# Kernel tuning notes

Hardware: AMD Instinct MI355X
Metric: run time of the kernel (lower is better)

Reference implementation:

```python
import jax, jax.numpy as jnp
import numpy as np

H = 256          # hidden_channels
R = 64           # num_rbf
N = 20000        # nodes
E = 320000       # edges
CUTOFF_LO = 0.0
CUTOFF_UP = 5.0
LN_EPS = 1e-5


def _layernorm(x, g, b):
    mu = jnp.mean(x, axis=-1, keepdims=True)
    var = jnp.var(x, axis=-1, keepdims=True)
    return (x - mu) * jax.lax.rsqrt(var + LN_EPS) * g + b


def _cosine_cutoff(r):
    # cutoff_lower == 0 branch of CosineCutoff
    c = 0.5 * (jnp.cos(r * (jnp.pi / CUTOFF_UP)) + 1.0)
    return c * (r < CUTOFF_UP).astype(r.dtype)


def setup_inputs() -> dict:
    key = jax.random.key(0)
    ks = jax.random.split(key, 16)
    def xavier(k, shape):
        fan_in, fan_out = shape[1], shape[0]
        lim = np.sqrt(6.0 / (fan_in + fan_out))
        return jax.random.uniform(k, shape, jnp.float32, -lim, lim)
    x = jax.random.normal(ks[0], (N, H), jnp.float32)
    edge_index = jax.random.randint(ks[1], (2, E), 0, N, jnp.int64)
    edge_weight = jax.random.uniform(ks[2], (E,), jnp.float32, 0.0, CUTOFF_UP)
    edge_attr = jax.random.normal(ks[3], (E, R), jnp.float32)
    return {
        "x": x,
        "edge_index": edge_index,
        "edge_weight": edge_weight,
        "edge_attr": edge_attr,
        "ln_g": jnp.ones((H,), jnp.float32),
        "ln_b": jnp.zeros((H,), jnp.float32),
        "Wq": xavier(ks[4], (H, H)), "bq": jnp.zeros((H,), jnp.float32),
        "Wk": xavier(ks[5], (H, H)), "bk": jnp.zeros((H,), jnp.float32),
        "Wv": xavier(ks[6], (H, H)), "bv": jnp.zeros((H,), jnp.float32),
        "Wo": xavier(ks[7], (H, H)), "bo": jnp.zeros((H,), jnp.float32),
        "Wdk": xavier(ks[8], (H, R)), "bdk": jnp.zeros((H,), jnp.float32),
        "Wdv": xavier(ks[9], (H, R)), "bdv": jnp.zeros((H,), jnp.float32),
    }


def reference(x, edge_index, edge_weight, edge_attr,
              ln_g, ln_b, Wq, bq, Wk, bk, Wv, bv, Wo, bo, Wdk, bdk, Wdv, bdv):
    src = edge_index[0]  # j (messages come from)
    dst = edge_index[1]  # i (messages aggregate to)

    x_norm = _layernorm(x, ln_g, ln_b)                     # [N,H]
    q = x_norm @ Wq.T + bq                                 # [N,H]
    k = x_norm @ Wk.T + bk
    v = x_norm @ Wv.T + bv

    dk = jax.nn.silu(edge_attr @ Wdk.T + bdk)              # [E,H]
    dv = jax.nn.silu(edge_attr @ Wdv.T + bdv)              # [E,H]

    q_i = q[dst]                                           # [E,H]
    k_j = k[src]
    v_j = v[src]

    attn = jnp.sum(q_i * k_j * dk, axis=1)                 # [E]
    attn = jax.nn.silu(attn) * _cosine_cutoff(edge_weight) # [E]

    msg = v_j * dv * attn[:, None]                         # [E,H]
    agg = jax.ops.segment_sum(msg, dst, num_segments=x.shape[0])  # [N,H]

    out = agg @ Wo.T + bo
    return x + out
```

## Files before the change

### kernel.cpp

```cpp
#include <hip/hip_runtime.h>
#include <math.h>

#define NN 20000
#define H 256
#define R 64
#define EE 320000
#define LN_EPS 1e-5f
#define NB 79

using short8  = __attribute__((ext_vector_type(8))) short;
using ushort8 = __attribute__((ext_vector_type(8))) unsigned short;
using f32x4   = __attribute__((ext_vector_type(4))) float;

typedef __attribute__((address_space(3))) unsigned int lds_uint;
typedef const __attribute__((address_space(1))) unsigned int glb_uint;

__device__ __forceinline__ float silu_f(float x) {
    return x * __builtin_amdgcn_rcpf(1.0f + __expf(-x));
}

__device__ __forceinline__ unsigned short f2bf(float f) {
    unsigned u = __float_as_uint(f);
    u += 0x7fff + ((u >> 16) & 1);
    return (unsigned short)(u >> 16);
}
__device__ __forceinline__ float bf2f(unsigned short s) {
    return __uint_as_float(((unsigned)s) << 16);
}
__device__ __forceinline__ unsigned short f2h(float f) {
    unsigned r;
    asm("v_cvt_f16_f32 %0, %1" : "=v"(r) : "v"(f));
    return (unsigned short)r;
}
__device__ __forceinline__ float h2f(unsigned short h) {
    float f;
    asm("v_cvt_f32_f16 %0, %1" : "=v"(f) : "v"((unsigned)h));
    return f;
}

__device__ __forceinline__ int sw_idx(int row, int col) {
    return row * 64 + ((((col >> 3) ^ (row & 7)) << 3) | (col & 7));
}
__device__ __forceinline__ int dh_idx(int row, int col) {
    return row * 128 + (col ^ (((row >> 2) & 3) << 4));
}

__global__ __launch_bounds__(256) void k_prep(
    const float* __restrict__ Wq, const float* __restrict__ Wk,
    const float* __restrict__ Wv, const float* __restrict__ Wo,
    const float* __restrict__ g,  const float* __restrict__ b,
    const float* __restrict__ bq, const float* __restrict__ bk, const float* __restrict__ bv,
    const float* __restrict__ Wdk, const float* __restrict__ Wdv,
    unsigned short* __restrict__ wqkv_p, unsigned short* __restrict__ wo_p,
    unsigned short* __restrict__ wdk_p,  unsigned short* __restrict__ wdv_p,
    float* __restrict__ bias3, int* __restrict__ hist)
{
    const int bid = blockIdx.x, t = threadIdx.x;
    if (bid < 128) {
        const int mat = bid >> 5;
        const float* W = mat == 0 ? Wq : (mat == 1 ? Wk : (mat == 2 ? Wv : Wo));
        unsigned short* out = (mat < 3) ? wqkv_p + (size_t)mat * 131072 : wo_p;
        const int fold = mat < 3;
        const int flat = (bid & 31) * 256 + t;
        const int tile = flat >> 9;
        const int rem  = flat & 511;
        const int ks   = rem >> 6;
        const int lane = rem & 63;
        const int nl = lane & 15, quad = lane >> 4;
        const int h  = tile * 16 + nl;
        const int c0 = ks * 32 + quad * 8;
        short8 hi8, lo8;
        #pragma unroll
        for (int j = 0; j < 8; ++j) {
            float wv = W[(size_t)h * 256 + c0 + j];
            if (fold) wv *= g[c0 + j];
            const unsigned short hh = f2bf(wv);
            hi8[j] = (short)hh;
            lo8[j] = (short)f2bf(wv - bf2f(hh));
        }
        unsigned short* ob = out + ((size_t)(tile * 8 + ks)) * 1024;
        *(short8*)&ob[lane * 8] = hi8;
        *(short8*)&ob[512 + lane * 8] = lo8;
    } else if (bid < 160) {
        const int flat = (bid - 128) * 256 + t;
        const int mat  = flat >> 12;
        const int rem  = flat & 4095;
        const int hh   = rem >> 11;
        const int r2   = rem & 2047;
        const int row  = r2 >> 4;
        const int col4 = (r2 & 15) * 4;
        const float* W = mat == 0 ? Wdk : Wdv;
        unsigned short* out = (mat == 0 ? wdk_p : wdv_p) + hh * 16384;
        const float4 w4 = *(const float4*)(W + (size_t)(hh * 128 + row) * 64 + col4);
        const unsigned short h0 = f2bf(w4.x), h1 = f2bf(w4.y), h2 = f2bf(w4.z), h3 = f2bf(w4.w);
        ushort4 hi4 = {h0, h1, h2, h3};
        ushort4 lo4 = {f2bf(w4.x - bf2f(h0)), f2bf(w4.y - bf2f(h1)),
                       f2bf(w4.z - bf2f(h2)), f2bf(w4.w - bf2f(h3))};
        const int di = sw_idx(row, col4);
        *(ushort4*)&out[di] = hi4;
        *(ushort4*)&out[8192 + di] = lo4;
    } else if (bid < 163) {
        const int mat = bid - 160, h = t;
        const float* W  = mat == 0 ? Wq : (mat == 1 ? Wk : Wv);
        const float* bb = mat == 0 ? bq : (mat == 1 ? bk : bv);
        float s = 0.f;
        const float* wr = W + (size_t)h * 256;
        for (int c = 0; c < 256; c += 4) {
            const float4 w4 = *(const float4*)(wr + c);
            const float4 b4 = *(const float4*)(b + c);
            s += w4.x * b4.x + w4.y * b4.y + w4.z * b4.z + w4.w * b4.w;
        }
        bias3[mat * 256 + h] = bb[h] + s;
    } else {
        const int i = (bid - 163) * 256 + t;
        if (i < NN) hist[i] = 0;
    }
}

__global__ __launch_bounds__(64, 2) void k_ln_qkv(
    const float* __restrict__ x,
    const unsigned short* __restrict__ wqkv_p, const float* __restrict__ bias3,
    float* __restrict__ q, float* __restrict__ k, float* __restrict__ v)
{
    const int t = threadIdx.x;
    const int lane = t & 63;
    const int nl = lane & 15, quad = lane >> 4;
    const int nbase = blockIdx.x * 16;
    const int node = nbase + nl;
    const bool nv = node < NN;

    float xv[64];
    float sum = 0.f, sq = 0.f;
    {
        const float* xp = x + (size_t)node * H + quad * 8;
        #pragma unroll
        for (int ks = 0; ks < 8; ++ks) {
            float4 x0 = {0.f,0.f,0.f,0.f}, x1 = {0.f,0.f,0.f,0.f};
            if (nv) {
                x0 = *(const float4*)(xp + ks * 32);
                x1 = *(const float4*)(xp + ks * 32 + 4);
            }
            xv[ks*8+0]=x0.x; xv[ks*8+1]=x0.y; xv[ks*8+2]=x0.z; xv[ks*8+3]=x0.w;
            xv[ks*8+4]=x1.x; xv[ks*8+5]=x1.y; xv[ks*8+6]=x1.z; xv[ks*8+7]=x1.w;
            sum += x0.x+x0.y+x0.z+x0.w + x1.x+x1.y+x1.z+x1.w;
            sq  += x0.x*x0.x+x0.y*x0.y+x0.z*x0.z+x0.w*x0.w
                 + x1.x*x1.x+x1.y*x1.y+x1.z*x1.z+x1.w*x1.w;
        }
    }
    sum += __shfl_xor(sum, 16); sum += __shfl_xor(sum, 32);
    sq  += __shfl_xor(sq, 16);  sq  += __shfl_xor(sq, 32);
    const float mu  = sum * (1.0f / H);
    const float var = sq * (1.0f / H) - mu * mu;
    const float rs  = rsqrtf(var + LN_EPS);

    short8 a_hi[8], a_lo[8];
    #pragma unroll
    for (int ks = 0; ks < 8; ++ks) {
        #pragma unroll
        for (int j = 0; j < 8; ++j) {
            const float z = (xv[ks*8+j] - mu) * rs;
            const unsigned short hh = f2bf(z);
            a_hi[ks][j] = (short)hh;
            a_lo[ks][j] = (short)f2bf(z - bf2f(hh));
        }
    }

    for (int mat = 0; mat < 3; ++mat) {
        float* outp = mat == 0 ? q : (mat == 1 ? k : v);
        const float* bp = bias3 + mat * 256;
        const unsigned short* wb = wqkv_p + (size_t)mat * 131072 + lane * 8;
        for (int tile = 0; tile < 16; ++tile) {
            const unsigned short* gb = wb + (size_t)tile * 8192;
            const float bbv = bp[tile * 16 + nl];
            f32x4 acc = {bbv, bbv, bbv, bbv};
            #pragma unroll
            for (int ks = 0; ks < 8; ++ks) {
                const short8 b_hi = *(const short8*)(gb + ks * 1024);
                const short8 b_lo = *(const short8*)(gb + ks * 1024 + 512);
                acc = __builtin_amdgcn_mfma_f32_16x16x32_bf16(a_hi[ks], b_hi, acc, 0, 0, 0);
                acc = __builtin_amdgcn_mfma_f32_16x16x32_bf16(a_lo[ks], b_hi, acc, 0, 0, 0);
                acc = __builtin_amdgcn_mfma_f32_16x16x32_bf16(a_hi[ks], b_lo, acc, 0, 0, 0);
            }
            #pragma unroll
            for (int r = 0; r < 4; ++r) {
                const int onode = nbase + quad * 4 + r;
                if (onode < NN)
                    outp[(size_t)onode * H + tile * 16 + nl] = acc[r];
            }
        }
    }
}

__global__ __launch_bounds__(256) void k_hist(const int* __restrict__ ei, int* __restrict__ hist) {
    int e = blockIdx.x * 256 + threadIdx.x;
    if (e < EE) atomicAdd(&hist[ei[EE + e]], 1);
}

__global__ __launch_bounds__(256) void k_scan1(const int* __restrict__ hist,
                                               int* __restrict__ cursor, int* __restrict__ bsum) {
    const int t = threadIdx.x, i = blockIdx.x * 256 + t;
    const int lane = t & 63, w = t >> 6;
    const int v = (i < NN) ? hist[i] : 0;
    int incl = v;
    #pragma unroll
    for (int off = 1; off < 64; off <<= 1) {
        int u = __shfl_up(incl, off);
        if (lane >= off) incl += u;
    }
    __shared__ int ws[4];
    if (lane == 63) ws[w] = incl;
    __syncthreads();
    int base = 0;
    #pragma unroll
    for (int j = 0; j < 4; ++j) if (j < w) base += ws[j];
    if (i < NN) cursor[i] = base + incl - v;
    if (t == 255) bsum[blockIdx.x] = base + incl;
}

__global__ __launch_bounds__(128) void k_scan2(int* __restrict__ bsum) {
    __shared__ int buf[128];
    const int t = threadIdx.x;
    const int v = (t < NB) ? bsum[t] : 0;
    buf[t] = v;
    __syncthreads();
    #pragma unroll
    for (int off = 1; off < 128; off <<= 1) {
        int add = (t >= off) ? buf[t - off] : 0;
        __syncthreads();
        buf[t] += add;
        __syncthreads();
    }
    if (t < NB) bsum[t] = buf[t] - v;
}

__global__ __launch_bounds__(256) void k_scatter(const int* __restrict__ ei,
                                                 int* __restrict__ cursor,
                                                 const int* __restrict__ bsum,
                                                 int* __restrict__ perm) {
    int e = blockIdx.x * 256 + threadIdx.x;
    if (e < EE) {
        int d = ei[EE + e];
        int pos = atomicAdd(&cursor[d], 1) + bsum[d >> 8];
        perm[pos] = e;
    }
}

__global__ __launch_bounds__(256, 3) void k_edge(
    const float* __restrict__ q, const float* __restrict__ k, const float* __restrict__ v,
    const int* __restrict__ ei, const float* __restrict__ ew, const float* __restrict__ ea,
    const unsigned short* __restrict__ wdk_p, const float* __restrict__ bdk,
    const unsigned short* __restrict__ wdv_p, const float* __restrict__ bdv,
    const int* __restrict__ perm,
    float* __restrict__ agg)
{
    __shared__ __align__(16) unsigned short w_region[2 * 128 * 64];
    __shared__ __align__(16) unsigned short dks_h[64 * 128];
    __shared__ float attn_s[64];
    __shared__ int src_s[64], dst_s[64];

    const unsigned short* w_hi_s = w_region;
    const unsigned short* w_lo_s = w_region + 128 * 64;

    const int t    = threadIdx.x;
    const int bi   = blockIdx.x;
    const int eb   = ((bi & 7) * 625 + (bi >> 3)) * 64;
    const int lane = t & 63, wave = t >> 6;
    const int nl   = lane & 15, quad = lane >> 4;
    const int estrip = wave * 16;
    const int tx = t & 31, ty = t >> 5;
    const int h0 = tx * 4, e0 = ty * 8;

    {
        const ushort8* sp = (const ushort8*)wdk_p + t;
        ushort8* dpw = (ushort8*)w_region + (t & 192);
        #pragma unroll
        for (int c = 0; c < 8; ++c)
            __builtin_amdgcn_global_load_lds((glb_uint*)(sp + c * 256),
                                             (lds_uint*)(dpw + c * 256), 16, 0, 0);
    }

    if (t < 64) {
        const int e = perm[eb + t];
        src_s[t] = ei[e];
        dst_s[t] = ei[EE + e];
        attn_s[t] = 0.f;
    }

    short8 a_hi[2], a_lo[2];
    {
        const int e = perm[eb + estrip + nl];
        const float* ap = ea + (size_t)e * R + quad * 8;
        #pragma unroll
        for (int ks = 0; ks < 2; ++ks) {
            const float4 x0 = *(const float4*)(ap + ks * 32);
            const float4 x1 = *(const float4*)(ap + ks * 32 + 4);
            const float zz[8] = {x0.x, x0.y, x0.z, x0.w, x1.x, x1.y, x1.z, x1.w};
            #pragma unroll
            for (int j = 0; j < 8; ++j) {
                const unsigned short hv = f2bf(zz[j]);
                a_hi[ks][j] = (short)hv;
                a_lo[ks][j] = (short)f2bf(zz[j] - bf2f(hv));
            }
        }
    }
    __syncthreads();

    for (int img = 0; img < 4; ++img) {
        const int hh = img & 1;

        if (img == 2 && t < 64) {
            const int e = perm[eb + t];
            const float rr = ew[e];
            const float cut = (rr < 5.0f) ? 0.5f * (__cosf(rr * 0.6283185307f) + 1.0f) : 0.0f;
            attn_s[t] = silu_f(attn_s[t]) * cut;
        }

        const float* bias = (img < 2) ? bdk : bdv;
        f32x4 accA[8];
        #pragma unroll
        for (int tt = 0; tt < 8; ++tt) {
            const int wrow = tt * 16 + nl;
            short8 b_hi[2], b_lo[2];
            #pragma unroll
            for (int ks = 0; ks < 2; ++ks) {
                const int idx = wrow * 64 + ((((ks * 4 + quad) ^ (nl & 7)) << 3));
                b_hi[ks] = *(const short8*)&w_hi_s[idx];
                b_lo[ks] = *(const short8*)&w_lo_s[idx];
            }
            const float bb = bias[hh * 128 + tt * 16 + nl];
            f32x4 acc = {bb, bb, bb, bb};
            #pragma unroll
            for (int ks = 0; ks < 2; ++ks) {
                acc = __builtin_amdgcn_mfma_f32_16x16x32_bf16(a_hi[ks], b_hi[ks], acc, 0, 0, 0);
                acc = __builtin_amdgcn_mfma_f32_16x16x32_bf16(a_lo[ks], b_hi[ks], acc, 0, 0, 0);
                acc = __builtin_amdgcn_mfma_f32_16x16x32_bf16(a_hi[ks], b_lo[ks], acc, 0, 0, 0);
            }
            accA[tt] = acc;
        }
        __syncthreads();

        if (img < 3) {
            const unsigned short* nip = (img == 0) ? wdk_p + 16384
                                      : (img == 1) ? wdv_p : wdv_p + 16384;
            const ushort8* sp = (const ushort8*)nip + t;
            ushort8* dpw = (ushort8*)w_region + (t & 192);
            #pragma unroll
            for (int c = 0; c < 8; ++c)
                __builtin_amdgcn_global_load_lds((glb_uint*)(sp + c * 256),
                                                 (lds_uint*)(dpw + c * 256), 16, 0, 0);
        }

        #pragma unroll
        for (int tt = 0; tt < 8; ++tt)
            #pragma unroll
            for (int r = 0; r < 4; ++r)
                dks_h[dh_idx(estrip + quad * 4 + r, tt * 16 + nl)] =
                    f2h(silu_f(accA[tt][r]));

        if (img < 2) {
            #pragma unroll
            for (int i = 0; i < 8; ++i) {
                const int d = dst_s[e0 + i], s = src_s[e0 + i];
                const float4 qi = *(const float4*)(q + (size_t)d * H + hh * 128 + h0);
                const float4 kj = *(const float4*)(k + (size_t)s * H + hh * 128 + h0);
                const ushort4 dk4 = *(const ushort4*)&dks_h[dh_idx(e0 + i, h0)];
                float part = qi.x * kj.x * h2f(dk4.x) + qi.y * kj.y * h2f(dk4.y)
                           + qi.z * kj.z * h2f(dk4.z) + qi.w * kj.w * h2f(dk4.w);
                #pragma unroll
                for (int off = 16; off; off >>= 1) part += __shfl_xor(part, off);
                if (tx == 0) attn_s[e0 + i] += part;
            }
        } else {
            float4 m = {0.f, 0.f, 0.f, 0.f};
            int cur_d = -1;
            #pragma unroll
            for (int i = 0; i < 8; ++i) {
                const int d = dst_s[e0 + i], s = src_s[e0 + i];
                const float a = attn_s[e0 + i];
                const float4 vj = *(const float4*)(v + (size_t)s * H + hh * 128 + h0);
                const ushort4 dv4 = *(const ushort4*)&dks_h[dh_idx(e0 + i, h0)];
                float4 mi;
                mi.x = vj.x * h2f(dv4.x) * a;
                mi.y = vj.y * h2f(dv4.y) * a;
                mi.z = vj.z * h2f(dv4.z) * a;
                mi.w = vj.w * h2f(dv4.w) * a;
                if (d != cur_d) {
                    if (cur_d >= 0) {
                        float* dp = agg + (size_t)cur_d * H + hh * 128 + h0;
                        atomicAdd(dp + 0, m.x); atomicAdd(dp + 1, m.y);
                        atomicAdd(dp + 2, m.z); atomicAdd(dp + 3, m.w);
                    }
                    m = mi; cur_d = d;
                } else {
                    m.x += mi.x; m.y += mi.y; m.z += mi.z; m.w += mi.w;
                }
            }
            {
                float* dp = agg + (size_t)cur_d * H + hh * 128 + h0;
                atomicAdd(dp + 0, m.x); atomicAdd(dp + 1, m.y);
                atomicAdd(dp + 2, m.z); atomicAdd(dp + 3, m.w);
            }
        }
        __syncthreads();
    }
}

__global__ __launch_bounds__(64, 2) void k_out(
    const float* __restrict__ aggm, const unsigned short* __restrict__ wo_p,
    const float* __restrict__ bo, const float* __restrict__ x, float* __restrict__ out)
{
    const int t = threadIdx.x;
    const int lane = t & 63;
    const int nl = lane & 15, quad = lane >> 4;
    const int nbase = blockIdx.x * 16;
    const int node = nbase + nl;
    const bool nv = node < NN;

    short8 a_hi[8], a_lo[8];
    {
        const float* ap = aggm + (size_t)node * H + quad * 8;
        #pragma unroll
        for (int ks = 0; ks < 8; ++ks) {
            float4 x0 = {0.f,0.f,0.f,0.f}, x1 = {0.f,0.f,0.f,0.f};
            if (nv) { x0 = *(const float4*)(ap + ks * 32); x1 = *(const float4*)(ap + ks * 32 + 4); }
            const float zz[8] = {x0.x,x0.y,x0.z,x0.w,x1.x,x1.y,x1.z,x1.w};
            #pragma unroll
            for (int j = 0; j < 8; ++j) {
                const unsigned short hh = f2bf(zz[j]);
                a_hi[ks][j] = (short)hh;
                a_lo[ks][j] = (short)f2bf(zz[j] - bf2f(hh));
            }
        }
    }
    for (int tile = 0; tile < 16; ++tile) {
        const unsigned short* gb = wo_p + (size_t)tile * 8192 + lane * 8;
        const float bbv = bo[tile * 16 + nl];
        f32x4 acc = {bbv, bbv, bbv, bbv};
        #pragma unroll
        for (int ks = 0; ks < 8; ++ks) {
            const short8 b_hi = *(const short8*)(gb + ks * 1024);
            const short8 b_lo = *(const short8*)(gb + ks * 1024 + 512);
            acc = __builtin_amdgcn_mfma_f32_16x16x32_bf16(a_hi[ks], b_hi, acc, 0, 0, 0);
            acc = __builtin_amdgcn_mfma_f32_16x16x32_bf16(a_lo[ks], b_hi, acc, 0, 0, 0);
            acc = __builtin_amdgcn_mfma_f32_16x16x32_bf16(a_hi[ks], b_lo, acc, 0, 0, 0);
        }
        #pragma unroll
        for (int r = 0; r < 4; ++r) {
            const int onode = nbase + quad * 4 + r;
            if (onode < NN) {
                const size_t oi = (size_t)onode * H + tile * 16 + nl;
                out[oi] = x[oi] + acc[r];
            }
        }
    }
}

extern "C" void kernel_launch(void* const* d_in, const int* in_sizes, int n_in,
                              void* d_out, int out_size, void* d_ws, size_t ws_size,
                              hipStream_t stream) {
    const float* x   = (const float*)d_in[0];
    const int*   ei  = (const int*)d_in[1];
    const float* ew  = (const float*)d_in[2];
    const float* ea  = (const float*)d_in[3];
    const float* g   = (const float*)d_in[4];
    const float* b   = (const float*)d_in[5];
    const float* Wq  = (const float*)d_in[6];  const float* bq  = (const float*)d_in[7];
    const float* Wk  = (const float*)d_in[8];  const float* bk  = (const float*)d_in[9];
    const float* Wv  = (const float*)d_in[10]; const float* bv  = (const float*)d_in[11];
    const float* Wo  = (const float*)d_in[12]; const float* bo  = (const float*)d_in[13];
    const float* Wdk = (const float*)d_in[14]; const float* bdk = (const float*)d_in[15];
    const float* Wdv = (const float*)d_in[16]; const float* bdv = (const float*)d_in[17];

    float* q    = (float*)d_ws;
    float* k    = q + (size_t)NN * H;
    float* v    = k + (size_t)NN * H;
    float* agg  = v + (size_t)NN * H;
    int*   hist = (int*)(agg + (size_t)NN * H);
    int*   cur  = hist + NN;
    int*   bsum = cur + NN;
    int*   perm = bsum + 128;
    unsigned short* wqkv_p = (unsigned short*)(perm + EE);
    unsigned short* wo_p   = wqkv_p + 393216;
    unsigned short* wdk_p  = wo_p + 131072;
    unsigned short* wdv_p  = wdk_p + 32768;
    float* bias3 = (float*)(wdv_p + 32768);

    hipMemsetAsync(agg, 0, (size_t)NN * H * sizeof(float), stream);
    k_prep<<<242, 256, 0, stream>>>(Wq, Wk, Wv, Wo, g, b, bq, bk, bv, Wdk, Wdv,
                                    wqkv_p, wo_p, wdk_p, wdv_p, bias3, hist);
    k_hist<<<EE / 256, 256, 0, stream>>>(ei, hist);
    k_ln_qkv<<<(NN + 15) / 16, 64, 0, stream>>>(x, wqkv_p, bias3, q, k, v);
    k_scan1<<<NB, 256, 0, stream>>>(hist, cur, bsum);
    k_scan2<<<1, 128, 0, stream>>>(bsum);
    k_scatter<<<EE / 256, 256, 0, stream>>>(ei, cur, bsum, perm);
    k_edge<<<EE / 64, 256, 0, stream>>>(q, k, v, ei, ew, ea, wdk_p, bdk, wdv_p, bdv, perm, agg);
    k_out<<<(NN + 15) / 16, 64, 0, stream>>>(agg, wo_p, bo, x, (float*)d_out);
}
```

Measured before the change: 647.8 us.

## Compute full-width dk/dv tiles in LDS and process both halves per gather pass

The edge kernel now computes both 128-column halves of the dk (and later dv) projection into a doubled LDS buffer before running a single gather pass. Each pass covers all 256 channels, which halves the number of attention and message loops and their barriers. It also reuses the q row across consecutive edges that share a destination, and merges the atomic flushes for the two halves. In exchange LDS use doubles and the launch bound drops from 3 to 2 blocks per CU, which lowers occupancy.

```diff
diff --git a/kernel.cpp b/kernel.cpp
--- a/kernel.cpp
+++ b/kernel.cpp
@@ -42,7 +42,7 @@
     return row * 64 + ((((col >> 3) ^ (row & 7)) << 3) | (col & 7));
 }
 __device__ __forceinline__ int dh_idx(int row, int col) {
-    return row * 128 + (col ^ (((row >> 2) & 3) << 4));
+    return row * 256 + (col ^ (((row >> 2) & 3) << 4));
 }
 
 __global__ __launch_bounds__(256) void k_prep(
@@ -245,7 +245,7 @@
     }
 }
 
-__global__ __launch_bounds__(256, 3) void k_edge(
+__global__ __launch_bounds__(256, 2) void k_edge(
     const float* __restrict__ q, const float* __restrict__ k, const float* __restrict__ v,
     const int* __restrict__ ei, const float* __restrict__ ew, const float* __restrict__ ea,
     const unsigned short* __restrict__ wdk_p, const float* __restrict__ bdk,
@@ -254,7 +254,7 @@
     float* __restrict__ agg)
 {
     __shared__ __align__(16) unsigned short w_region[2 * 128 * 64];
-    __shared__ __align__(16) unsigned short dks_h[64 * 128];
+    __shared__ __align__(16) unsigned short dks_h[64 * 256];
     __shared__ float attn_s[64];
     __shared__ int src_s[64], dst_s[64];
 
@@ -292,9 +292,9 @@
         const float* ap = ea + (size_t)e * R + quad * 8;
         #pragma unroll
         for (int ks = 0; ks < 2; ++ks) {
-            const float4 x0 = *(const float4*)(ap + ks * 32);
-            const float4 x1 = *(const float4*)(ap + ks * 32 + 4);
-            const float zz[8] = {x0.x, x0.y, x0.z, x0.w, x1.x, x1.y, x1.z, x1.w};
+            const f32x4 x0 = *(const f32x4*)(ap + ks * 32);
+            const f32x4 x1 = *(const f32x4*)(ap + ks * 32 + 4);
+            const float zz[8] = {x0[0], x0[1], x0[2], x0[3], x1[0], x1[1], x1[2], x1[3]};
             #pragma unroll
             for (int j = 0; j < 8; ++j) {
                 const unsigned short hv = f2bf(zz[j]);
@@ -305,17 +305,50 @@
     }
     __syncthreads();
 
-    for (int img = 0; img < 4; ++img) {
-        const int hh = img & 1;
-
-        if (img == 2 && t < 64) {
-            const int e = perm[eb + t];
-            const float rr = ew[e];
-            const float cut = (rr < 5.0f) ? 0.5f * (__cosf(rr * 0.6283185307f) + 1.0f) : 0.0f;
-            attn_s[t] = silu_f(attn_s[t]) * cut;
-        }
-
-        const float* bias = (img < 2) ? bdk : bdv;
+    #define MFMA_TO_DKS(BIAS, HALF)                                                   \
+    {                                                                                 \
+        f32x4 accA[8];                                                                \
+        _Pragma("unroll")                                                             \
+        for (int tt = 0; tt < 8; ++tt) {                                              \
+            const int wrow = tt * 16 + nl;                                            \
+            short8 b_hi[2], b_lo[2];                                                  \
+            _Pragma("unroll")                                                         \
+            for (int ks = 0; ks < 2; ++ks) {                                          \
+                const int idx = wrow * 64 + ((((ks * 4 + quad) ^ (nl & 7)) << 3));    \
+                b_hi[ks] = *(const short8*)&w_hi_s[idx];                              \
+                b_lo[ks] = *(const short8*)&w_lo_s[idx];                              \
+            }                                                                         \
+            const float bb = (BIAS)[(HALF) * 128 + tt * 16 + nl];                     \
+            f32x4 acc = {bb, bb, bb, bb};                                             \
+            _Pragma("unroll")                                                         \
+            for (int ks = 0; ks < 2; ++ks) {                                          \
+                acc = __builtin_amdgcn_mfma_f32_16x16x32_bf16(a_hi[ks], b_hi[ks], acc, 0, 0, 0); \
+                acc = __builtin_amdgcn_mfma_f32_16x16x32_bf16(a_lo[ks], b_hi[ks], acc, 0, 0, 0); \
+                acc = __builtin_amdgcn_mfma_f32_16x16x32_bf16(a_hi[ks], b_lo[ks], acc, 0, 0, 0); \
+            }                                                                         \
+            accA[tt] = acc;                                                           \
+        }                                                                             \
+        __syncthreads();                         \
+                   \
+        _Pragma("unroll")                                                             \
+        for (int tt = 0; tt < 8; ++tt)                                                \
+            _Pragma("unroll")                                                         \
+            for (int r = 0; r < 4; ++r)                                               \
+                dks_h[dh_idx(estrip + quad * 4 + r, (HALF) * 128 + tt * 16 + nl)] =   \
+                    f2h(silu_f(accA[tt][r]));                                         \
+    }
+
+    #define STAGE(PTR)                                                                \
+    {                                                                                 \
+        const ushort8* sp = (const ushort8*)(PTR) + t;                                \
+        ushort8* dpw = (ushort8*)w_region + (t & 192);                                \
+        _Pragma("unroll")                                                             \
+        for (int c = 0; c < 8; ++c)                                                   \
+            __builtin_amdgcn_global_load_lds((glb_uint*)(sp + c * 256),               \
+                                             (lds_uint*)(dpw + c * 256), 16, 0, 0);   \
+    }
+
+    {
         f32x4 accA[8];
         #pragma unroll
         for (int tt = 0; tt < 8; ++tt) {
@@ -327,7 +360,7 @@
                 b_hi[ks] = *(const short8*)&w_hi_s[idx];
                 b_lo[ks] = *(const short8*)&w_lo_s[idx];
             }
-            const float bb = bias[hh * 128 + tt * 16 + nl];
+            const float bb = bdk[tt * 16 + nl];
             f32x4 acc = {bb, bb, bb, bb};
             #pragma unroll
             for (int ks = 0; ks < 2; ++ks) {
@@ -338,71 +371,97 @@
             accA[tt] = acc;
         }
         __syncthreads();
-
-        if (img < 3) {
-            const unsigned short* nip = (img == 0) ? wdk_p + 16384
-                                      : (img == 1) ? wdv_p : wdv_p + 16384;
-            const ushort8* sp = (const ushort8*)nip + t;
-            ushort8* dpw = (ushort8*)w_region + (t & 192);
-            #pragma unroll
-            for (int c = 0; c < 8; ++c)
-                __builtin_amdgcn_global_load_lds((glb_uint*)(sp + c * 256),
-                                                 (lds_uint*)(dpw + c * 256), 16, 0, 0);
-        }
-
+        STAGE(wdk_p + 16384);
         #pragma unroll
         for (int tt = 0; tt < 8; ++tt)
             #pragma unroll
             for (int r = 0; r < 4; ++r)
                 dks_h[dh_idx(estrip + quad * 4 + r, tt * 16 + nl)] =
                     f2h(silu_f(accA[tt][r]));
-
-        if (img < 2) {
-            #pragma unroll
-            for (int i = 0; i < 8; ++i) {
-                const int d = dst_s[e0 + i], s = src_s[e0 + i];
-                const float4 qi = *(const float4*)(q + (size_t)d * H + hh * 128 + h0);
-                const float4 kj = *(const float4*)(k + (size_t)s * H + hh * 128 + h0);
-                const ushort4 dk4 = *(const ushort4*)&dks_h[dh_idx(e0 + i, h0)];
-                float part = qi.x * kj.x * h2f(dk4.x) + qi.y * kj.y * h2f(dk4.y)
-                           + qi.z * kj.z * h2f(dk4.z) + qi.w * kj.w * h2f(dk4.w);
-                #pragma unroll
-                for (int off = 16; off; off >>= 1) part += __shfl_xor(part, off);
-                if (tx == 0) attn_s[e0 + i] += part;
-            }
-        } else {
-            float4 m = {0.f, 0.f, 0.f, 0.f};
-            int cur_d = -1;
-            #pragma unroll
-            for (int i = 0; i < 8; ++i) {
-                const int d = dst_s[e0 + i], s = src_s[e0 + i];
-                const float a = attn_s[e0 + i];
-                const float4 vj = *(const float4*)(v + (size_t)s * H + hh * 128 + h0);
-                const ushort4 dv4 = *(const ushort4*)&dks_h[dh_idx(e0 + i, h0)];
-                float4 mi;
-                mi.x = vj.x * h2f(dv4.x) * a;
-                mi.y = vj.y * h2f(dv4.y) * a;
-                mi.z = vj.z * h2f(dv4.z) * a;
-                mi.w = vj.w * h2f(dv4.w) * a;
-                if (d != cur_d) {
-                    if (cur_d >= 0) {
-                        float* dp = agg + (size_t)cur_d * H + hh * 128 + h0;
-                        atomicAdd(dp + 0, m.x); atomicAdd(dp + 1, m.y);
-                        atomicAdd(dp + 2, m.z); atomicAdd(dp + 3, m.w);
-                    }
-                    m = mi; cur_d = d;
-                } else {
-                    m.x += mi.x; m.y += mi.y; m.z += mi.z; m.w += mi.w;
+    }
+    __syncthreads();
+    MFMA_TO_DKS(bdk, 1);
+    STAGE(wdv_p);
+
+    {
+        float4 qi0 = {0.f,0.f,0.f,0.f}, qi1 = {0.f,0.f,0.f,0.f};
+        int pd = -1;
+        #pragma unroll
+        for (int i = 0; i < 8; ++i) {
+            const int d = dst_s[e0 + i], s = src_s[e0 + i];
+            if (d != pd) {
+                qi0 = *(const float4*)(q + (size_t)d * H + h0);
+                qi1 = *(const float4*)(q + (size_t)d * H + 128 + h0);
+                pd = d;
+            }
+            const float4 kj0 = *(const float4*)(k + (size_t)s * H + h0);
+            const float4 kj1 = *(const float4*)(k + (size_t)s * H + 128 + h0);
+            const ushort4 d40 = *(const ushort4*)&dks_h[dh_idx(e0 + i, h0)];
+            const ushort4 d41 = *(const ushort4*)&dks_h[dh_idx(e0 + i, 128 + h0)];
+            float part = qi0.x * kj0.x * h2f(d40.x) + qi0.y * kj0.y * h2f(d40.y)
+                       + qi0.z * kj0.z * h2f(d40.z) + qi0.w * kj0.w * h2f(d40.w)
+                       + qi1.x * kj1.x * h2f(d41.x) + qi1.y * kj1.y * h2f(d41.y)
+                       + qi1.z * kj1.z * h2f(d41.z) + qi1.w * kj1.w * h2f(d41.w);
+            #pragma unroll
+            for (int off = 16; off; off >>= 1) part += __shfl_xor(part, off);
+            if (tx == 0) attn_s[e0 + i] += part;
+        }
+    }
+    __syncthreads();
+
+    if (t < 64) {
+        const int e = perm[eb + t];
+        const float rr = ew[e];
+        const float cut = (rr < 5.0f) ? 0.5f * (__cosf(rr * 0.6283185307f) + 1.0f) : 0.0f;
+        attn_s[t] = silu_f(attn_s[t]) * cut;
+    }
+
+    MFMA_TO_DKS(bdv, 0);
+    STAGE(wdv_p + 16384);
+    __syncthreads();
+    MFMA_TO_DKS(bdv, 1);
+
+    {
+        float4 m0 = {0.f,0.f,0.f,0.f}, m1 = {0.f,0.f,0.f,0.f};
+        int cur_d = -1;
+        #pragma unroll
+        for (int i = 0; i < 8; ++i) {
+            const int d = dst_s[e0 + i], s = src_s[e0 + i];
+            const float a = attn_s[e0 + i];
+            const float4 vj0 = *(const float4*)(v + (size_t)s * H + h0);
+            const float4 vj1 = *(const float4*)(v + (size_t)s * H + 128 + h0);
+            const ushort4 d40 = *(const ushort4*)&dks_h[dh_idx(e0 + i, h0)];
+            const ushort4 d41 = *(const ushort4*)&dks_h[dh_idx(e0 + i, 128 + h0)];
+            if (d != cur_d) {
+                if (cur_d >= 0) {
+                    float* dp = agg + (size_t)cur_d * H;
+                    atomicAdd(dp + h0 + 0, m0.x); atomicAdd(dp + h0 + 1, m0.y);
+                    atomicAdd(dp + h0 + 2, m0.z); atomicAdd(dp + h0 + 3, m0.w);
+                    atomicAdd(dp + 128 + h0 + 0, m1.x); atomicAdd(dp + 128 + h0 + 1, m1.y);
+                    atomicAdd(dp + 128 + h0 + 2, m1.z); atomicAdd(dp + 128 + h0 + 3, m1.w);
                 }
-            }
-            {
-                float* dp = agg + (size_t)cur_d * H + hh * 128 + h0;
-                atomicAdd(dp + 0, m.x); atomicAdd(dp + 1, m.y);
-                atomicAdd(dp + 2, m.z); atomicAdd(dp + 3, m.w);
-            }
-        }
-        __syncthreads();
-    }
+                m0.x = vj0.x * h2f(d40.x) * a; m0.y = vj0.y * h2f(d40.y) * a;
+                m0.z = vj0.z * h2f(d40.z) * a; m0.w = vj0.w * h2f(d40.w) * a;
+                m1.x = vj1.x * h2f(d41.x) * a; m1.y = vj1.y * h2f(d41.y) * a;
+                m1.z = vj1.z * h2f(d41.z) * a; m1.w = vj1.w * h2f(d41.w) * a;
+                cur_d = d;
+            } else {
+                m0.x += vj0.x * h2f(d40.x) * a; m0.y += vj0.y * h2f(d40.y) * a;
+                m0.z += vj0.z * h2f(d40.z) * a; m0.w += vj0.w * h2f(d40.w) * a;
+                m1.x += vj1.x * h2f(d41.x) * a; m1.y += vj1.y * h2f(d41.y) * a;
+                m1.z += vj1.z * h2f(d41.z) * a; m1.w += vj1.w * h2f(d41.w) * a;
+            }
+        }
+        {
+            float* dp = agg + (size_t)cur_d * H;
+            atomicAdd(dp + h0 + 0, m0.x); atomicAdd(dp + h0 + 1, m0.y);
+            atomicAdd(dp + h0 + 2, m0.z); atomicAdd(dp + h0 + 3, m0.w);
+            atomicAdd(dp + 128 + h0 + 0, m1.x); atomicAdd(dp + 128 + h0 + 1, m1.y);
+            atomicAdd(dp + 128 + h0 + 2, m1.z); atomicAdd(dp + 128 + h0 + 3, m1.w);
+        }
+    }
+    #undef MFMA_TO_DKS
+    #undef STAGE
 }
 
 __global__ __launch_bounds__(64, 2) void k_out(
```

After: 630.1 us. -2.7%, faster.
